# Kernel tuning notes

Hardware: AMD Instinct MI355X
Metric: run time of the kernel (lower is better)

Reference implementation:

```python
import jax, jax.numpy as jnp
import numpy as np

NUM_GRAPHS = 10000
N_NODES = 1000000
FEAT = 128

def setup_inputs() -> dict:
    key = jax.random.key(0)
    k1, k2 = jax.random.split(key)
    h_t = jax.random.normal(k1, (N_NODES, FEAT), dtype=jnp.float32)
    batch = jnp.sort(jax.random.randint(k2, (N_NODES,), 0, NUM_GRAPHS, dtype=jnp.int64))
    return {"h_t": h_t, "batch": batch}

def reference(h_t, batch):
    # The original shuffles node features *within* each graph before sum-pooling.
    # Sum pooling is permutation-invariant, so the per-graph randperm shuffle is a
    # no-op mathematically: output == segment_sum(h_t, batch).
    # This fuses the whole per-graph loop into a single scatter-add.
    return jax.ops.segment_sum(h_t, batch, num_segments=NUM_GRAPHS)
```

## Files before the change

kernel.cpp:

```cpp
#include <hip/hip_runtime.h>


#define FEAT 128
#define ROWS_PER_WAVE 256

__global__ __launch_bounds__(256) void segsum_kernel(
    const float* __restrict__ h,
    const int* __restrict__ batch,
    float* __restrict__ out,
    int n_rows) {
  const int wave = (blockIdx.x * blockDim.x + threadIdx.x) >> 6;
  const int lane = threadIdx.x & 63;

  long long row0 = (long long)wave * ROWS_PER_WAVE;
  if (row0 >= n_rows) return;
  long long row_end = row0 + ROWS_PER_WAVE;
  if (row_end > n_rows) row_end = n_rows;

  const int col = lane * 2;

  float2 acc;
  acc.x = 0.0f;
  acc.y = 0.0f;
  int cur = batch[row0];

  for (long long r = row0; r < row_end; ++r) {
    const int b = batch[r];
    const float2 v = *(const float2*)(h + r * (long long)FEAT + col);
    if (b != cur) {
      float* dst = out + (long long)cur * FEAT + col;
      atomicAdd(dst + 0, acc.x);
      atomicAdd(dst + 1, acc.y);
      acc.x = 0.0f;
      acc.y = 0.0f;
      cur = b;
    }
    acc.x += v.x;
    acc.y += v.y;
  }
  {
    float* dst = out + (long long)cur * FEAT + col;
    atomicAdd(dst + 0, acc.x);
    atomicAdd(dst + 1, acc.y);
  }
}

extern "C" void kernel_launch(void* const* d_in, const int* in_sizes, int n_in,
                              void* d_out, int out_size, void* d_ws, size_t ws_size,
                              hipStream_t stream) {
  const float* h_t = (const float*)d_in[0];
  const int* batch = (const int*)d_in[1];
  float* out = (float*)d_out;
  const int n_rows = in_sizes[1];

  hipMemsetAsync(d_out, 0, (size_t)out_size * sizeof(float), stream);

  const int n_waves = (n_rows + ROWS_PER_WAVE - 1) / ROWS_PER_WAVE;
  const int block = 256;
  const int waves_per_block = block / 64;
  const int grid = (n_waves + waves_per_block - 1) / waves_per_block;

  segsum_kernel<<<grid, block, 0, stream>>>(h_t, batch, out, n_rows);
}
```

Baseline: 695.3 us.

## Split wave into two half-waves with float4 nontemporal loads and 16-row unroll

Each wave now splits into two 32-lane halves that handle alternating rows, with each lane loading float4 through nontemporal loads. Batch indices are read as int4 vectors, and the main loop is unrolled to keep eight row loads in flight. Rows per wave drop from 256 to 128 to add parallelism. The aim is to raise memory-level parallelism and bandwidth use on a streaming read. In exchange it roughly doubles the atomic flushes, since both half-waves flush at every segment boundary, and adds tail-handling code.

```diff
diff --git a/kernel.cpp b/kernel.cpp
--- a/kernel.cpp
+++ b/kernel.cpp
@@ -2,7 +2,13 @@
 
 
 #define FEAT 128
-#define ROWS_PER_WAVE 256
+#define ROWS_PER_WAVE 128
+
+typedef float vfloat4 __attribute__((ext_vector_type(4)));
+
+static __device__ inline vfloat4 ntload4(const float* p) {
+  return __builtin_nontemporal_load((const vfloat4*)p);
+}
 
 __global__ __launch_bounds__(256) void segsum_kernel(
     const float* __restrict__ h,
@@ -11,37 +17,79 @@
     int n_rows) {
   const int wave = (blockIdx.x * blockDim.x + threadIdx.x) >> 6;
   const int lane = threadIdx.x & 63;
+  const int sub = lane >> 5;
+  const int col = (lane & 31) * 4;
 
   long long row0 = (long long)wave * ROWS_PER_WAVE;
   if (row0 >= n_rows) return;
   long long row_end = row0 + ROWS_PER_WAVE;
   if (row_end > n_rows) row_end = n_rows;
 
-  const int col = lane * 2;
+  vfloat4 acc = {0.0f, 0.0f, 0.0f, 0.0f};
+  long long first = row0 + sub;
+  int cur = batch[first < n_rows ? first : (n_rows - 1)];
 
-  float2 acc;
-  acc.x = 0.0f;
-  acc.y = 0.0f;
-  int cur = batch[row0];
+#define STEP(B, V)                                        \
+  {                                                       \
+    const int b_ = (B);                                   \
+    if (b_ != cur) {          \
+      float* dst = out + (long long)cur * FEAT + col;     \
+      atomicAdd(dst + 0, acc.x);                          \
+      atomicAdd(dst + 1, acc.y);                          \
+      atomicAdd(dst + 2, acc.z);                          \
+      atomicAdd(dst + 3, acc.w);                          \
+      acc.x = 0.0f; acc.y = 0.0f;                         \
+      acc.z = 0.0f; acc.w = 0.0f;                         \
+      cur = b_;                                           \
+    }                                                     \
+    acc.x += (V).x; acc.y += (V).y;                       \
+    acc.z += (V).z; acc.w += (V).w;                       \
+  }
 
-  for (long long r = row0; r < row_end; ++r) {
+  long long r = row0;
+  for (; r + 16 <= row_end; r += 16) {
+    const int4 ba = *(const int4*)(batch + r);
+    const int4 bb = *(const int4*)(batch + r + 4);
+    const int4 bc = *(const int4*)(batch + r + 8);
+    const int4 bd = *(const int4*)(batch + r + 12);
+    const float* hp = h + (r + sub) * (long long)FEAT + col;
+    vfloat4 v0 = ntload4(hp + 0 * 2 * FEAT);
+    vfloat4 v1 = ntload4(hp + 1 * 2 * FEAT);
+    vfloat4 v2 = ntload4(hp + 2 * 2 * FEAT);
+    vfloat4 v3 = ntload4(hp + 3 * 2 * FEAT);
+    vfloat4 v4 = ntload4(hp + 4 * 2 * FEAT);
+    vfloat4 v5 = ntload4(hp + 5 * 2 * FEAT);
+    vfloat4 v6 = ntload4(hp + 6 * 2 * FEAT);
+    vfloat4 v7 = ntload4(hp + 7 * 2 * FEAT);
+
+    STEP(sub ? ba.y : ba.x, v0)
+    STEP(sub ? ba.w : ba.z, v1)
+    STEP(sub ? bb.y : bb.x, v2)
+    STEP(sub ? bb.w : bb.z, v3)
+    STEP(sub ? bc.y : bc.x, v4)
+    STEP(sub ? bc.w : bc.z, v5)
+    STEP(sub ? bd.y : bd.x, v6)
+    STEP(sub ? bd.w : bd.z, v7)
+  }
+
+  for (; r + 2 <= row_end; r += 2) {
+    const int b = batch[r + sub];
+    const vfloat4 v = *(const vfloat4*)(h + (r + sub) * (long long)FEAT + col);
+    STEP(b, v)
+  }
+  if (r < row_end && sub == 0) {
     const int b = batch[r];
-    const float2 v = *(const float2*)(h + r * (long long)FEAT + col);
-    if (b != cur) {
-      float* dst = out + (long long)cur * FEAT + col;
-      atomicAdd(dst + 0, acc.x);
-      atomicAdd(dst + 1, acc.y);
-      acc.x = 0.0f;
-      acc.y = 0.0f;
-      cur = b;
-    }
-    acc.x += v.x;
-    acc.y += v.y;
+    const vfloat4 v = *(const vfloat4*)(h + r * (long long)FEAT + col);
+    STEP(b, v)
   }
+#undef STEP
+
   {
     float* dst = out + (long long)cur * FEAT + col;
     atomicAdd(dst + 0, acc.x);
     atomicAdd(dst + 1, acc.y);
+    atomicAdd(dst + 2, acc.z);
+    atomicAdd(dst + 3, acc.w);
   }
 }
 
```

Result: faster. 636.4 us (-8.5%).
